# Kernel optimization log

Measured on AMD Instinct MI355X. Metric: run time of the kernel, lower is better.

## Reference

```python
import jax, jax.numpy as jnp
import numpy as np

DIM = 768
HEADS = 12
B, N = 1, 4096


def setup_inputs() -> dict:
    key = jax.random.key(0)
    k1, k2, k3 = jax.random.split(key, 3)
    x = jax.random.normal(k1, (B, N, DIM), dtype=jnp.float32)
    W_qkv = jax.random.normal(k2, (DIM, 3 * DIM), dtype=jnp.float32) * (DIM ** -0.5)
    W_out = jax.random.normal(k3, (DIM, DIM), dtype=jnp.float32) * (DIM ** -0.5)
    b_out = jnp.zeros((DIM,), dtype=jnp.float32)
    return {"x": x, "W_qkv": W_qkv, "W_out": W_out, "b_out": b_out}


def reference(x, W_qkv, W_out, b_out):
    b, n, dim = x.shape
    h = HEADS
    d = dim // h
    qkv = x @ W_qkv  # [b, n, 3*dim]
    q, k, v = jnp.split(qkv, 3, axis=-1)
    # 'b n (h d) -> b h n d'
    def to_heads(a):
        return a.reshape(b, n, h, d).transpose(0, 2, 1, 3)
    q, k, v = to_heads(q), to_heads(k), to_heads(v)
    # NOTE: original module computes self.scale but never applies it -> unscaled dots
    dots = jnp.einsum('bhid,bhjd->bhij', q, k)
    attn = jax.nn.softmax(dots, axis=-1)
    out = jnp.einsum('bhij,bhjd->bhid', attn, v)
    out = out.transpose(0, 2, 1, 3).reshape(b, n, dim)  # 'b h n d -> b n (h d)'
    return out @ W_out + b_out
```

## Files before the change

kernel.cpp:

```cpp
#include <hip/hip_runtime.h>

typedef unsigned short ushort_t;
typedef unsigned int uint_t;
typedef __bf16 bf16x8 __attribute__((ext_vector_type(8)));
typedef __bf16 bf16x4 __attribute__((ext_vector_type(4)));
typedef float f32x4 __attribute__((ext_vector_type(4)));
typedef ushort_t u16x4 __attribute__((ext_vector_type(4)));

#define NSEQ 4096
#define DIMM 768
#define NQKV 2304
#define HEADS 12
#define LOG2E 1.4426950408889634f

#if __has_builtin(__builtin_amdgcn_exp2f)
#define EXP2(x) __builtin_amdgcn_exp2f(x)
#else
#define EXP2(x) exp2f(x)
#endif


__device__ __forceinline__ ushort_t f2bf(float f) {
    uint_t u = __float_as_uint(f);
    u = u + 0x7fffu + ((u >> 16) & 1u);
    return (ushort_t)(u >> 16);
}
__device__ __forceinline__ f32x4 zero4() {
    f32x4 v = {0.f, 0.f, 0.f, 0.f};
    return v;
}

__device__ __forceinline__ void pack_w_tile(const float* __restrict__ src,
                                            ushort_t* __restrict__ dst,
                                            int K, int N, int bk, int bn, int t,
                                            ushort_t* Ls) {
    const int tr = t >> 4, tc = t & 15;
#pragma unroll
    for (int i = 0; i < 4; ++i) {
        int r = tr + 16 * i;
        float4 v = *(const float4*)(&src[(size_t)(bk + r) * N + bn + tc * 4]);
        const float* vv = (const float*)&v;
#pragma unroll
        for (int j = 0; j < 4; ++j) Ls[(tc * 4 + j) * 72 + r] = f2bf(vv[j]);
    }
    __syncthreads();
    const int KB = K >> 3;
    const int n = t >> 2;
    const int ks = t & 3;
    const int gn = bn + n;
    size_t base = ((size_t)(gn >> 4) * KB + ((bk + ks * 16) >> 3)) * 128 + (gn & 15) * 8;
    *(uint4*)(&dst[base])       = *(const uint4*)(&Ls[n * 72 + ks * 16]);
    *(uint4*)(&dst[base + 128]) = *(const uint4*)(&Ls[n * 72 + ks * 16 + 8]);
}

#define CVT_BLOCKS   3072
#define PW1_BLOCKS   (12 * 36)
#define PW2_BLOCKS   (12 * 12)

__global__ __launch_bounds__(256) void prep_kernel(
    const float* __restrict__ X, const float* __restrict__ Wqkv, const float* __restrict__ Wout,
    ushort_t* __restrict__ Ap, ushort_t* __restrict__ Wqp, ushort_t* __restrict__ Wop)
{
    __shared__ ushort_t Ls[64 * 72];
    const int b = blockIdx.x;
    const int t = threadIdx.x;
    if (b < CVT_BLOCKS) {
        int i = b * 256 + t;
        int row = i / (DIMM / 4);
        int k0 = (i - row * (DIMM / 4)) * 4;
        float4 v = *(const float4*)(&X[(size_t)row * DIMM + k0]);
        u16x4 p = { f2bf(v.x), f2bf(v.y), f2bf(v.z), f2bf(v.w) };
        size_t idx = ((size_t)(row >> 4) * (DIMM / 8) + (k0 >> 3)) * 128 + (row & 15) * 8 + (k0 & 7);
        *(u16x4*)(&Ap[idx]) = p;
    } else if (b < CVT_BLOCKS + PW1_BLOCKS) {
        int j = b - CVT_BLOCKS;
        pack_w_tile(Wqkv, Wqp, DIMM, NQKV, (j % 12) * 64, (j / 12) * 64, t, Ls);
    } else {
        int j = b - CVT_BLOCKS - PW1_BLOCKS;
        pack_w_tile(Wout, Wop, DIMM, DIMM, (j % 12) * 64, (j / 12) * 64, t, Ls);
    }
}

#define QKV_LOAD(af, bfv, kt) do {                                                            \
    _Pragma("unroll")                                                                         \
    for (int mi = 0; mi < 4; ++mi)                                                            \
        af[mi] = *(const bf16x8*)(&Ap[((size_t)(amb + mi) * KB + (kt) * 4 + g) * 128 + m16 * 8]); \
    _Pragma("unroll")                                                                         \
    for (int nj = 0; nj < 4; ++nj)                                                            \
        bfv[nj] = *(const bf16x8*)(&Bp[((size_t)(bnb + nj) * KB + (kt) * 4 + g) * 128 + m16 * 8]); \
} while (0)

__global__ __launch_bounds__(256) void qkv_gemm_kernel(
    const ushort_t* __restrict__ Ap, const ushort_t* __restrict__ Bp,
    ushort_t* __restrict__ Qp, ushort_t* __restrict__ Kp, ushort_t* __restrict__ Vp)
{
    const int t = threadIdx.x;
    const int lane = t & 63;
    const int w = t >> 6;
    const int m16 = lane & 15;
    const int g = lane >> 4;
    const int wrow = (w >> 1) * 64;
    const int wcol = (w & 1) * 64;
    const int bm = blockIdx.y * 128;
    const int bn = blockIdx.x * 128;
    const int amb = (bm + wrow) >> 4;
    const int bnb = (bn + wcol) >> 4;
    const int KB = DIMM / 8;
    const int which = bn / DIMM;

    f32x4 acc[4][4];
#pragma unroll
    for (int i = 0; i < 4; ++i)
#pragma unroll
        for (int j = 0; j < 4; ++j) acc[i][j] = zero4();

    bf16x8 af0[4], bf0[4], af1[4], bf1[4];
    QKV_LOAD(af0, bf0, 0);

    if (which < 2) {
        for (int kt = 0; kt < 24; kt += 2) {
            QKV_LOAD(af1, bf1, kt + 1);
#pragma unroll
            for (int mi = 0; mi < 4; ++mi)
#pragma unroll
                for (int nj = 0; nj < 4; ++nj)
                    acc[mi][nj] = __builtin_amdgcn_mfma_f32_16x16x32_bf16(bf0[nj], af0[mi], acc[mi][nj], 0, 0, 0);
            if (kt + 2 < 24) QKV_LOAD(af0, bf0, kt + 2);
#pragma unroll
            for (int mi = 0; mi < 4; ++mi)
#pragma unroll
                for (int nj = 0; nj < 4; ++nj)
                    acc[mi][nj] = __builtin_amdgcn_mfma_f32_16x16x32_bf16(bf1[nj], af1[mi], acc[mi][nj], 0, 0, 0);
        }
        ushort_t* dst = (which == 0) ? Qp : Kp;
        const float scale = (which == 0) ? LOG2E : 1.0f;
        const int cb = bn - which * DIMM + wcol;
        const int h = cb >> 6;
        const int ghi = g >> 1, glo = g & 1;
#pragma unroll
        for (int mi = 0; mi < 4; ++mi) {
            int sblk = amb + mi;
#pragma unroll
            for (int nj = 0; nj < 4; ++nj) {
                size_t idx = (((size_t)h * 256 + sblk) * 8 + nj * 2 + ghi) * 128 + m16 * 8 + glo * 4;
                u16x4 pk = { f2bf(acc[mi][nj][0] * scale), f2bf(acc[mi][nj][1] * scale),
                             f2bf(acc[mi][nj][2] * scale), f2bf(acc[mi][nj][3] * scale) };
                *(u16x4*)(&dst[idx]) = pk;
            }
        }
    } else {
        for (int kt = 0; kt < 24; kt += 2) {
            QKV_LOAD(af1, bf1, kt + 1);
#pragma unroll
            for (int mi = 0; mi < 4; ++mi)
#pragma unroll
                for (int nj = 0; nj < 4; ++nj)
                    acc[mi][nj] = __builtin_amdgcn_mfma_f32_16x16x32_bf16(af0[mi], bf0[nj], acc[mi][nj], 0, 0, 0);
            if (kt + 2 < 24) QKV_LOAD(af0, bf0, kt + 2);
#pragma unroll
            for (int mi = 0; mi < 4; ++mi)
#pragma unroll
                for (int nj = 0; nj < 4; ++nj)
                    acc[mi][nj] = __builtin_amdgcn_mfma_f32_16x16x32_bf16(af1[mi], bf1[nj], acc[mi][nj], 0, 0, 0);
        }
        const int cb = bn - 2 * DIMM + wcol;
        const int h = cb >> 6;
        const int ghi = g >> 1, glo = g & 1;
        const int kb8 = (bm + wrow) >> 3;
#pragma unroll
        for (int mi = 0; mi < 4; ++mi) {
#pragma unroll
            for (int nj = 0; nj < 4; ++nj) {
                size_t idx = (((size_t)h * 512 + kb8 + mi * 2 + ghi) * 4 + nj) * 128 + m16 * 8 + glo * 4;
                u16x4 pk = { f2bf(acc[mi][nj][0]), f2bf(acc[mi][nj][1]),
                             f2bf(acc[mi][nj][2]), f2bf(acc[mi][nj][3]) };
                *(u16x4*)(&Vp[idx]) = pk;
            }
        }
    }
}

#define ATTN_LOADK(dst, ptr) do {                          \
    dst[0][0] = *(const bf16x8*)(ptr);                     \
    dst[0][1] = *(const bf16x8*)((ptr) + 512);             \
    dst[1][0] = *(const bf16x8*)((ptr) + 1024);            \
    dst[1][1] = *(const bf16x8*)((ptr) + 1536);            \
} while (0)

#define ATTN_LOADV(dst, ptr) do {                          \
    dst[0] = *(const bf16x8*)(ptr);                        \
    dst[1] = *(const bf16x8*)((ptr) + 128);                \
    dst[2] = *(const bf16x8*)((ptr) + 256);                \
    dst[3] = *(const bf16x8*)((ptr) + 384);                \
} while (0)

#define ATTN_COMPUTE(KF, VF) do {                                                             \
    _Pragma("unroll")                                                                         \
    for (int mi = 0; mi < 2; ++mi) {                                                          \
        _Pragma("unroll")                                                                     \
        for (int nj = 0; nj < 2; ++nj) {                                                      \
            f32x4 st = zero4();                                                               \
            st = __builtin_amdgcn_mfma_f32_16x16x32_bf16(KF[nj][0], qf[mi][0], st, 0, 0, 0);  \
            st = __builtin_amdgcn_mfma_f32_16x16x32_bf16(KF[nj][1], qf[mi][1], st, 0, 0, 0);  \
            bf16x4 pk = { (__bf16)EXP2(st[0]), (__bf16)EXP2(st[1]),                           \
                          (__bf16)EXP2(st[2]), (__bf16)EXP2(st[3]) };                         \
            *(bf16x4*)(&Ps[w][(mi * 16 + m16) * 40 + nj * 16 + g * 4]) = pk;                  \
        }                                                                                     \
        bf16x8 pf = *(const bf16x8*)(&Ps[w][(mi * 16 + m16) * 40 + g * 8]);                   \
        lfrag[mi] = __builtin_amdgcn_mfma_f32_16x16x32_bf16(pf, onesf, lfrag[mi], 0, 0, 0);   \
        _Pragma("unroll")                                                                     \
        for (int dj = 0; dj < 4; ++dj)                                                        \
            oacc[mi][dj] = __builtin_amdgcn_mfma_f32_16x16x32_bf16(pf, VF[dj], oacc[mi][dj], 0, 0, 0); \
    }                                                                                         \
} while (0)

__global__ __launch_bounds__(256, 3) void attn_kernel(
    const ushort_t* __restrict__ Qp, const ushort_t* __restrict__ Kp,
    const ushort_t* __restrict__ Vp, float* __restrict__ Opart, float* __restrict__ Lpart,
    int niter)
{
    __shared__ ushort_t Ps[4][32 * 40];
    const int t = threadIdx.x;
    const int lane = t & 63;
    const int w = t >> 6;
    const int m16 = lane & 15;
    const int g = lane >> 4;
    const int h = blockIdx.y;
    const int half = blockIdx.z;
    const int qb = blockIdx.x * 128 + w * 32;
    const int qblk0 = qb >> 4;
    const int kblk0 = half * niter * 4;
    const int vblk0 = half * niter * 8;

    bf16x8 qf[2][2];
#pragma unroll
    for (int mi = 0; mi < 2; ++mi)
#pragma unroll
        for (int kd = 0; kd < 2; ++kd)
            qf[mi][kd] = *(const bf16x8*)(&Qp[(((size_t)h * 256 + qblk0 + mi) * 8 + kd * 4 + g) * 128 + m16 * 8]);

    const ushort_t* kp = Kp + ((size_t)h * 256 + kblk0) * 1024 + g * 128 + m16 * 8;
    const ushort_t* vp = Vp + ((size_t)h * 512 + vblk0) * 512 + g * 512 + m16 * 8;

    bf16x8 onesf;
#pragma unroll
    for (int i = 0; i < 8; ++i) onesf[i] = (__bf16)1.0f;

    f32x4 oacc[2][4];
#pragma unroll
    for (int mi = 0; mi < 2; ++mi)
#pragma unroll
        for (int dj = 0; dj < 4; ++dj) oacc[mi][dj] = zero4();
    f32x4 lfrag[2] = {zero4(), zero4()};

    bf16x8 ka[2][2], kb[2][2], va[4], vb[4];
    ATTN_LOADK(ka, kp); kp += 2048;
    ATTN_LOADV(va, vp); vp += 2048;
    asm volatile("" ::: "memory");

    const int nsteps = niter * 2;
    for (int s = 0; s < nsteps; s += 2) {
        ATTN_LOADK(kb, kp); kp += 2048;
        ATTN_LOADV(vb, vp); vp += 2048;
        asm volatile("" ::: "memory");
        ATTN_COMPUTE(ka, va);
        ATTN_LOADK(ka, kp); kp += 2048;
        ATTN_LOADV(va, vp); vp += 2048;
        asm volatile("" ::: "memory");
        ATTN_COMPUTE(kb, vb);
    }

    float* Oph = Opart + (size_t)half * NSEQ * DIMM;
    float* Lph = Lpart + (size_t)half * HEADS * NSEQ + (size_t)h * NSEQ;
    if (m16 == 0) {
#pragma unroll
        for (int mi = 0; mi < 2; ++mi)
#pragma unroll
            for (int r = 0; r < 4; ++r)
                Lph[qb + mi * 16 + g * 4 + r] = lfrag[mi][r];
    }
#pragma unroll
    for (int mi = 0; mi < 2; ++mi) {
#pragma unroll
        for (int r = 0; r < 4; ++r) {
            int row = qb + mi * 16 + g * 4 + r;
#pragma unroll
            for (int dj = 0; dj < 4; ++dj)
                Oph[(size_t)row * DIMM + h * 64 + dj * 16 + m16] = oacc[mi][dj][r];
        }
    }
}

__global__ __launch_bounds__(256) void merge_kernel(
    const float* __restrict__ Opart, const float* __restrict__ Lpart,
    ushort_t* __restrict__ Xap, int nsplit)
{
    int i = blockIdx.x * 256 + threadIdx.x;
    int row = i / (DIMM / 4);
    int col0 = (i - row * (DIMM / 4)) * 4;
    int h = col0 >> 6;
    float l = 0.f;
    f32x4 o = zero4();
    for (int s = 0; s < nsplit; ++s) {
        l += Lpart[(size_t)s * HEADS * NSEQ + (size_t)h * NSEQ + row];
        f32x4 ov = *(const f32x4*)(&Opart[(size_t)s * NSEQ * DIMM + (size_t)row * DIMM + col0]);
        o += ov;
    }
    float inv = 1.0f / l;
    u16x4 p = { f2bf(o[0] * inv), f2bf(o[1] * inv), f2bf(o[2] * inv), f2bf(o[3] * inv) };
    size_t idx = ((size_t)(row >> 4) * (DIMM / 8) + (col0 >> 3)) * 128 + (row & 15) * 8 + (col0 & 7);
    *(u16x4*)(&Xap[idx]) = p;
}

__global__ __launch_bounds__(64, 4) void out_gemm_kernel(
    const ushort_t* __restrict__ Ap, const ushort_t* __restrict__ Bp,
    const float* __restrict__ bias, float* __restrict__ out)
{
    const int lane = threadIdx.x & 63;
    const int m16 = lane & 15;
    const int g = lane >> 4;
    const int bm = blockIdx.y * 32;
    const int bn = blockIdx.x * 64;
    const int amb = bm >> 4;
    const int bnb = bn >> 4;
    const int KB = DIMM / 8;

    f32x4 acc[2][4];
#pragma unroll
    for (int i = 0; i < 2; ++i)
#pragma unroll
        for (int j = 0; j < 4; ++j) acc[i][j] = zero4();

#pragma unroll 2
    for (int kt = 0; kt < 24; ++kt) {
        bf16x8 af[2], bfv[4];
#pragma unroll
        for (int mi = 0; mi < 2; ++mi)
            af[mi] = *(const bf16x8*)(&Ap[((size_t)(amb + mi) * KB + kt * 4 + g) * 128 + m16 * 8]);
#pragma unroll
        for (int nj = 0; nj < 4; ++nj)
            bfv[nj] = *(const bf16x8*)(&Bp[((size_t)(bnb + nj) * KB + kt * 4 + g) * 128 + m16 * 8]);
#pragma unroll
        for (int mi = 0; mi < 2; ++mi)
#pragma unroll
            for (int nj = 0; nj < 4; ++nj)
                acc[mi][nj] = __builtin_amdgcn_mfma_f32_16x16x32_bf16(af[mi], bfv[nj], acc[mi][nj], 0, 0, 0);
    }
#pragma unroll
    for (int mi = 0; mi < 2; ++mi) {
#pragma unroll
        for (int nj = 0; nj < 4; ++nj) {
            int col = bn + nj * 16 + m16;
            float bv = bias[col];
#pragma unroll
            for (int r = 0; r < 4; ++r) {
                int row = bm + mi * 16 + g * 4 + r;
                out[(size_t)row * DIMM + col] = acc[mi][nj][r] + bv;
            }
        }
    }
}

extern "C" void kernel_launch(void* const* d_in, const int* in_sizes, int n_in,
                              void* d_out, int out_size, void* d_ws, size_t ws_size,
                              hipStream_t stream) {
    (void)in_sizes; (void)n_in; (void)out_size;
    const float* X    = (const float*)d_in[0];
    const float* Wqkv = (const float*)d_in[1];
    const float* Wout = (const float*)d_in[2];
    const float* bout = (const float*)d_in[3];
    float* out = (float*)d_out;

    const size_t TSZ = (size_t)NSEQ * DIMM;
    const size_t fixed = TSZ * 2 * 5 + (size_t)NQKV * DIMM * 2 + (size_t)DIMM * DIMM * 2;
    const size_t per_split = TSZ * 4 + (size_t)HEADS * NSEQ * 4;
    const int nsplit = (ws_size >= fixed + 4 * per_split) ? 4 : 2;

    unsigned char* p = (unsigned char*)d_ws;
    ushort_t* Ap  = (ushort_t*)p; p += TSZ * 2;
    ushort_t* Wqp = (ushort_t*)p; p += (size_t)NQKV * DIMM * 2;
    ushort_t* Wop = (ushort_t*)p; p += (size_t)DIMM * DIMM * 2;
    ushort_t* Qp  = (ushort_t*)p; p += TSZ * 2;
    ushort_t* Kp  = (ushort_t*)p; p += TSZ * 2;
    ushort_t* Vp  = (ushort_t*)p; p += TSZ * 2;
    ushort_t* Xap = (ushort_t*)p; p += TSZ * 2;
    float* Opart  = (float*)p;    p += (size_t)nsplit * TSZ * 4;
    float* Lpart  = (float*)p;

    const int niter = (NSEQ / 64) / nsplit;

    prep_kernel<<<CVT_BLOCKS + PW1_BLOCKS + PW2_BLOCKS, 256, 0, stream>>>(X, Wqkv, Wout, Ap, Wqp, Wop);
    qkv_gemm_kernel<<<dim3(NQKV / 128, NSEQ / 128), 256, 0, stream>>>(Ap, Wqp, Qp, Kp, Vp);
    attn_kernel<<<dim3(NSEQ / 128, HEADS, nsplit), 256, 0, stream>>>(Qp, Kp, Vp, Opart, Lpart, niter);
    merge_kernel<<<TSZ / 4 / 256, 256, 0, stream>>>(Opart, Lpart, Xap, nsplit);
    out_gemm_kernel<<<dim3(DIMM / 64, NSEQ / 32), 64, 0, stream>>>(Xap, Wop, bout, out);
}
```

Before: 199.7 us.

## Give each attention wave 64 query rows and sum softmax denominators in fp32

The attention kernel now runs 2 waves per block instead of 4, and each wave handles 64 query rows. Each loaded K/V tile is therefore reused across twice as many queries, halving global K/V traffic per query. The row-sum is now accumulated in fp32 registers and reduced with lane shuffles at the end, replacing the extra MFMA against a ones vector. The explicit double-buffered K/V prefetch is dropped in favour of a single load per step, which may expose memory latency, and the larger accumulators raise register pressure.

```diff
diff --git a/kernel.cpp b/kernel.cpp
--- a/kernel.cpp
+++ b/kernel.cpp
@@ -194,32 +194,12 @@
     dst[3] = *(const bf16x8*)((ptr) + 384);                \
 } while (0)
 
-#define ATTN_COMPUTE(KF, VF) do {                                                             \
-    _Pragma("unroll")                                                                         \
-    for (int mi = 0; mi < 2; ++mi) {                                                          \
-        _Pragma("unroll")                                                                     \
-        for (int nj = 0; nj < 2; ++nj) {                                                      \
-            f32x4 st = zero4();                                                               \
-            st = __builtin_amdgcn_mfma_f32_16x16x32_bf16(KF[nj][0], qf[mi][0], st, 0, 0, 0);  \
-            st = __builtin_amdgcn_mfma_f32_16x16x32_bf16(KF[nj][1], qf[mi][1], st, 0, 0, 0);  \
-            bf16x4 pk = { (__bf16)EXP2(st[0]), (__bf16)EXP2(st[1]),                           \
-                          (__bf16)EXP2(st[2]), (__bf16)EXP2(st[3]) };                         \
-            *(bf16x4*)(&Ps[w][(mi * 16 + m16) * 40 + nj * 16 + g * 4]) = pk;                  \
-        }                                                                                     \
-        bf16x8 pf = *(const bf16x8*)(&Ps[w][(mi * 16 + m16) * 40 + g * 8]);                   \
-        lfrag[mi] = __builtin_amdgcn_mfma_f32_16x16x32_bf16(pf, onesf, lfrag[mi], 0, 0, 0);   \
-        _Pragma("unroll")                                                                     \
-        for (int dj = 0; dj < 4; ++dj)                                                        \
-            oacc[mi][dj] = __builtin_amdgcn_mfma_f32_16x16x32_bf16(pf, VF[dj], oacc[mi][dj], 0, 0, 0); \
-    }                                                                                         \
-} while (0)
-
-__global__ __launch_bounds__(256, 3) void attn_kernel(
+__global__ __launch_bounds__(128, 3) void attn_kernel(
     const ushort_t* __restrict__ Qp, const ushort_t* __restrict__ Kp,
     const ushort_t* __restrict__ Vp, float* __restrict__ Opart, float* __restrict__ Lpart,
     int niter)
 {
-    __shared__ ushort_t Ps[4][32 * 40];
+    __shared__ ushort_t Ps[2][64 * 40];
     const int t = threadIdx.x;
     const int lane = t & 63;
     const int w = t >> 6;
@@ -227,14 +207,14 @@
     const int g = lane >> 4;
     const int h = blockIdx.y;
     const int half = blockIdx.z;
-    const int qb = blockIdx.x * 128 + w * 32;
+    const int qb = blockIdx.x * 128 + w * 64;
     const int qblk0 = qb >> 4;
     const int kblk0 = half * niter * 4;
     const int vblk0 = half * niter * 8;
 
-    bf16x8 qf[2][2];
-#pragma unroll
-    for (int mi = 0; mi < 2; ++mi)
+    bf16x8 qf[4][2];
+#pragma unroll
+    for (int mi = 0; mi < 4; ++mi)
 #pragma unroll
         for (int kd = 0; kd < 2; ++kd)
             qf[mi][kd] = *(const bf16x8*)(&Qp[(((size_t)h * 256 + qblk0 + mi) * 8 + kd * 4 + g) * 128 + m16 * 8]);
@@ -242,45 +222,51 @@
     const ushort_t* kp = Kp + ((size_t)h * 256 + kblk0) * 1024 + g * 128 + m16 * 8;
     const ushort_t* vp = Vp + ((size_t)h * 512 + vblk0) * 512 + g * 512 + m16 * 8;
 
-    bf16x8 onesf;
-#pragma unroll
-    for (int i = 0; i < 8; ++i) onesf[i] = (__bf16)1.0f;
-
-    f32x4 oacc[2][4];
-#pragma unroll
-    for (int mi = 0; mi < 2; ++mi)
+    f32x4 oacc[4][4];
+#pragma unroll
+    for (int mi = 0; mi < 4; ++mi)
 #pragma unroll
         for (int dj = 0; dj < 4; ++dj) oacc[mi][dj] = zero4();
-    f32x4 lfrag[2] = {zero4(), zero4()};
-
-    bf16x8 ka[2][2], kb[2][2], va[4], vb[4];
-    ATTN_LOADK(ka, kp); kp += 2048;
-    ATTN_LOADV(va, vp); vp += 2048;
-    asm volatile("" ::: "memory");
+    f32x4 lacc[4] = {zero4(), zero4(), zero4(), zero4()};
 
     const int nsteps = niter * 2;
-    for (int s = 0; s < nsteps; s += 2) {
-        ATTN_LOADK(kb, kp); kp += 2048;
-        ATTN_LOADV(vb, vp); vp += 2048;
+    for (int s = 0; s < nsteps; ++s) {
+        bf16x8 kf[2][2], vf[4];
+        ATTN_LOADK(kf, kp); kp += 2048;
+        ATTN_LOADV(vf, vp); vp += 2048;
         asm volatile("" ::: "memory");
-        ATTN_COMPUTE(ka, va);
-        ATTN_LOADK(ka, kp); kp += 2048;
-        ATTN_LOADV(va, vp); vp += 2048;
-        asm volatile("" ::: "memory");
-        ATTN_COMPUTE(kb, vb);
+#pragma unroll
+        for (int mi = 0; mi < 4; ++mi) {
+#pragma unroll
+            for (int nj = 0; nj < 2; ++nj) {
+                f32x4 st = zero4();
+                st = __builtin_amdgcn_mfma_f32_16x16x32_bf16(kf[nj][0], qf[mi][0], st, 0, 0, 0);
+                st = __builtin_amdgcn_mfma_f32_16x16x32_bf16(kf[nj][1], qf[mi][1], st, 0, 0, 0);
+                f32x4 p;
+#pragma unroll
+                for (int r = 0; r < 4; ++r) p[r] = EXP2(st[r]);
+                lacc[mi] += p;
+                bf16x4 pk = { (__bf16)p[0], (__bf16)p[1], (__bf16)p[2], (__bf16)p[3] };
+                *(bf16x4*)(&Ps[w][(mi * 16 + m16) * 40 + nj * 16 + g * 4]) = pk;
+            }
+            bf16x8 pf = *(const bf16x8*)(&Ps[w][(mi * 16 + m16) * 40 + g * 8]);
+#pragma unroll
+            for (int dj = 0; dj < 4; ++dj)
+                oacc[mi][dj] = __builtin_amdgcn_mfma_f32_16x16x32_bf16(pf, vf[dj], oacc[mi][dj], 0, 0, 0);
+        }
     }
 
     float* Oph = Opart + (size_t)half * NSEQ * DIMM;
     float* Lph = Lpart + (size_t)half * HEADS * NSEQ + (size_t)h * NSEQ;
-    if (m16 == 0) {
-#pragma unroll
-        for (int mi = 0; mi < 2; ++mi)
-#pragma unroll
-            for (int r = 0; r < 4; ++r)
-                Lph[qb + mi * 16 + g * 4 + r] = lfrag[mi][r];
-    }
-#pragma unroll
-    for (int mi = 0; mi < 2; ++mi) {
+#pragma unroll
+    for (int mi = 0; mi < 4; ++mi) {
+        float l = (lacc[mi][0] + lacc[mi][1]) + (lacc[mi][2] + lacc[mi][3]);
+        l += __shfl_xor(l, 16);
+        l += __shfl_xor(l, 32);
+        if (g == 0) Lph[qb + mi * 16 + m16] = l;
+    }
+#pragma unroll
+    for (int mi = 0; mi < 4; ++mi) {
 #pragma unroll
         for (int r = 0; r < 4; ++r) {
             int row = qb + mi * 16 + g * 4 + r;
@@ -391,7 +377,7 @@
 
     prep_kernel<<<CVT_BLOCKS + PW1_BLOCKS + PW2_BLOCKS, 256, 0, stream>>>(X, Wqkv, Wout, Ap, Wqp, Wop);
     qkv_gemm_kernel<<<dim3(NQKV / 128, NSEQ / 128), 256, 0, stream>>>(Ap, Wqp, Qp, Kp, Vp);
-    attn_kernel<<<dim3(NSEQ / 128, HEADS, nsplit), 256, 0, stream>>>(Qp, Kp, Vp, Opart, Lpart, niter);
+    attn_kernel<<<dim3(NSEQ / 128, HEADS, nsplit), 128, 0, stream>>>(Qp, Kp, Vp, Opart, Lpart, niter);
     merge_kernel<<<TSZ / 4 / 256, 256, 0, stream>>>(Opart, Lpart, Xap, nsplit);
     out_gemm_kernel<<<dim3(DIMM / 64, NSEQ / 32), 64, 0, stream>>>(Xap, Wop, bout, out);
 }
```

Result: faster. 195.8 us (-2.0%).
